# Kernel tuning notes

Hardware: AMD Instinct MI355X
Metric: run time of the kernel (lower is better)

Reference implementation:

```python
import jax, jax.numpy as jnp
import numpy as np

B = 4096
OBS_DIM = 1024
E_OUT = 512
H1 = 2048
H2 = 2048


def setup_inputs() -> dict:
    key = jax.random.key(0)
    ks = jax.random.split(key, 12)
    def kaiming(k, shape, fan_in):
        return jax.random.normal(k, shape, dtype=jnp.float32) * np.float32(np.sqrt(2.0 / fan_in))
    obs = jax.random.normal(ks[0], (B, OBS_DIM), dtype=jnp.float32)
    # lineare: Linear(obs_dim, e_outputs), torch weight shape [out, in]
    We = kaiming(ks[1], (E_OUT, OBS_DIM), OBS_DIM)
    be = jax.random.normal(ks[2], (E_OUT,), dtype=jnp.float32) * 0.01
    # obs_dim attention heads, each Linear(e_outputs, 2), stacked
    attn_W = kaiming(ks[3], (OBS_DIM, E_OUT, 2), E_OUT)
    attn_b = jax.random.normal(ks[4], (OBS_DIM, 2), dtype=jnp.float32) * 0.01
    # v_net: Linear(obs_dim,H1)+tanh, Linear(H1,H2)+[dropout(eval:no-op)]+tanh, Linear(H2,1)
    W1 = kaiming(ks[5], (H1, OBS_DIM), OBS_DIM)
    b1 = jnp.zeros((H1,), dtype=jnp.float32)
    W2 = kaiming(ks[6], (H2, H1), H1)
    b2 = jnp.zeros((H2,), dtype=jnp.float32)
    W3 = kaiming(ks[7], (1, H2), H2)
    b3 = jnp.zeros((1,), dtype=jnp.float32)
    return {"obs": obs, "We": We, "be": be, "attn_W": attn_W, "attn_b": attn_b,
            "W1": W1, "b1": b1, "W2": W2, "b2": b2, "W3": W3, "b3": b3}


def reference(obs, We, be, attn_W, attn_b, W1, b1, W2, b2, W3, b3):
    # e = tanh(lineare(obs)) : [B, E_OUT]
    e = jnp.tanh(obs @ We.T + be)
    # all obs_dim attention heads batched into one contraction: [B, OBS_DIM, 2]
    logits = jnp.einsum('be,oec->boc', e, attn_W) + attn_b
    # softmax over the 2 logits, keep prob of class 1 -> Attention [B, OBS_DIM]
    attention = jax.nn.softmax(logits, axis=-1)[..., 1]
    state_attention = obs * attention
    # v_net (eval mode: dropout is identity)
    h = jnp.tanh(state_attention @ W1.T + b1)
    h = jnp.tanh(h @ W2.T + b2)
    v = jnp.squeeze(h @ W3.T + b3, -1)  # [B]
    return (v, attention)
```

## Files before the change

### kernel.cpp

```cpp
#include <hip/hip_runtime.h>
#include <hip/hip_bf16.h>

typedef unsigned short u16;
typedef u16 u16x4 __attribute__((ext_vector_type(4)));
typedef u16 u16x8 __attribute__((ext_vector_type(8)));
typedef __bf16 bf16x8 __attribute__((ext_vector_type(8)));
typedef float f32x4 __attribute__((ext_vector_type(4)));

__device__ __forceinline__ u16 f2bf(float f) {
  unsigned u = __float_as_uint(f);
  u += 0x7FFFu + ((u >> 16) & 1u);
  return (u16)(u >> 16);
}
__device__ __forceinline__ float bf2f(u16 h) {
  return __uint_as_float(((unsigned)h) << 16);
}
__device__ __forceinline__ float tanh_fast(float x) {
  float t = __expf(2.0f * x);
  return 1.0f - 2.0f / (t + 1.0f);
}
__device__ __forceinline__ float sigmoid_fast(float x) {
  return 1.0f / (1.0f + __expf(-x));
}

__device__ __forceinline__ void glds16(const u16* g, u16* l) {
  __builtin_amdgcn_global_load_lds(
      (const __attribute__((address_space(1))) unsigned int*)g,
      (__attribute__((address_space(3))) unsigned int*)l, 16, 0, 0);
}

__device__ __forceinline__ void cvt4(const float* __restrict__ s, u16* __restrict__ d, int q) {
  float4 v = ((const float4*)s)[q];
  u16x4 o = { f2bf(v.x), f2bf(v.y), f2bf(v.z), f2bf(v.w) };
  ((u16x4*)d)[q] = o;
}

__global__ __launch_bounds__(256)
void prep_kernel(const float* __restrict__ obs, const float* __restrict__ We,
                 const float* __restrict__ W1, const float* __restrict__ W2,
                 const float* __restrict__ aW, const float* __restrict__ ab,
                 u16* __restrict__ obs_b, u16* __restrict__ We_b,
                 u16* __restrict__ W1_b, u16* __restrict__ W2_b,
                 u16* __restrict__ Wd, float* __restrict__ bd,
                 float* __restrict__ vzero) {
  int q = blockIdx.x * 256 + threadIdx.x;
  if (q < 1024) ((float4*)vzero)[q] = (float4){0.f, 0.f, 0.f, 0.f};
  if (q < 1048576) { cvt4(obs, obs_b, q); return; }
  q -= 1048576;
  if (q < 131072) { cvt4(We, We_b, q); return; }
  q -= 131072;
  if (q < 524288) { cvt4(W1, W1_b, q); return; }
  q -= 524288;
  if (q < 1048576) { cvt4(W2, W2_b, q); return; }
  q -= 1048576;
  if (q < 131072) {
    int i0 = q * 4;
    int o = i0 >> 9, e0 = i0 & 511;
    const float* p = aW + (size_t)o * 1024 + e0 * 2;
    float4 v0 = *(const float4*)p;
    float4 v1 = *(const float4*)(p + 4);
    u16x4 od = { f2bf(v0.y - v0.x), f2bf(v0.w - v0.z),
                 f2bf(v1.y - v1.x), f2bf(v1.w - v1.z) };
    *(u16x4*)(Wd + i0) = od;
    if (q < 256) {
      float4 a0 = *(const float4*)(ab + q * 8);
      float4 a1 = *(const float4*)(ab + q * 8 + 4);
      float4 ob = { a0.y - a0.x, a0.w - a0.z, a1.y - a1.x, a1.w - a1.z };
      *(float4*)(bd + q * 4) = ob;
    }
  }
}

template <int BM, int BN, int EP>
__global__ __launch_bounds__(256, 2)
void gemm_bt(const u16* __restrict__ A, const u16* __restrict__ Bt,
             int N, int K,
             const float* __restrict__ bias,
             u16* __restrict__ outb, float* __restrict__ outf,
             const u16* __restrict__ obsb, u16* __restrict__ sa,
             const float* __restrict__ W3, const float* __restrict__ b3,
             float* __restrict__ vout) {
  constexpr int CA = BM / 32;
  constexpr int CB = BN / 32;
  constexpr int MI = BM / 32;
  constexpr int NJ = BN / 32;

  __shared__ __align__(16) u16 As0[BM * 64];
  __shared__ __align__(16) u16 Bs0[BN * 64];
  __shared__ __align__(16) u16 As1[BM * 64];
  __shared__ __align__(16) u16 Bs1[BN * 64];

  const int tid = threadIdx.x;
  const int lane = tid & 63;
  const int wave = tid >> 6;
  const int bm = blockIdx.x, bn = blockIdx.y;

  const int r0 = tid >> 3;
  const int kcs = ((tid & 7) ^ (r0 & 7)) * 8;

  const u16* gA = A + (size_t)(bm * BM + r0) * K + kcs;
  const u16* gB = Bt + (size_t)(bn * BN + r0) * K + kcs;

  const int wm = (wave >> 1) * (BM / 2);
  const int wn = (wave & 1) * (BN / 2);
  const int fr = lane & 15;
  const int hi = lane >> 4;
  const int frx = fr & 7;

  f32x4 acc[MI][NJ];
#pragma unroll
  for (int i = 0; i < MI; ++i)
#pragma unroll
    for (int j = 0; j < NJ; ++j)
      acc[i][j] = (f32x4){0.f, 0.f, 0.f, 0.f};

  auto stage = [&](u16* __restrict__ dA, u16* __restrict__ dB) {
#pragma unroll
    for (int q = 0; q < CA; ++q)
      glds16(gA + (size_t)q * 32 * K, dA + tid * 8 + q * 2048);
#pragma unroll
    for (int q = 0; q < CB; ++q)
      glds16(gB + (size_t)q * 32 * K, dB + tid * 8 + q * 2048);
    gA += 64; gB += 64;
  };

  auto compute = [&](const u16* sA, const u16* sB) {
#pragma unroll
    for (int s = 0; s < 2; ++s) {
      const int ck = ((s * 4 + hi) ^ frx) * 8;
      bf16x8 a[MI], b[NJ];
#pragma unroll
      for (int i = 0; i < MI; ++i)
        a[i] = *(const bf16x8*)(sA + (wm + i * 16 + fr) * 64 + ck);
#pragma unroll
      for (int j = 0; j < NJ; ++j)
        b[j] = *(const bf16x8*)(sB + (wn + j * 16 + fr) * 64 + ck);
#pragma unroll
      for (int i = 0; i < MI; ++i)
#pragma unroll
        for (int j = 0; j < NJ; ++j)
          acc[i][j] = __builtin_amdgcn_mfma_f32_16x16x32_bf16(a[i], b[j], acc[i][j], 0, 0, 0);
    }
  };

  const int T = K >> 6;
  stage(As0, Bs0);
  __syncthreads();
  for (int k = 0; k < T; k += 2) {
    stage(As1, Bs1);
    compute(As0, Bs0);
    __syncthreads();
    if (k + 2 < T) stage(As0, Bs0);
    compute(As1, Bs1);
    __syncthreads();
  }

  if constexpr (EP == 2) {
    float vpart[MI][4];
#pragma unroll
    for (int i = 0; i < MI; ++i)
#pragma unroll
      for (int r = 0; r < 4; ++r) vpart[i][r] = 0.f;
#pragma unroll
    for (int j = 0; j < NJ; ++j) {
      const int col = bn * BN + wn + j * 16 + fr;
      const float bv = bias[col];
      const float w3 = W3[col];
#pragma unroll
      for (int i = 0; i < MI; ++i)
#pragma unroll
        for (int r = 0; r < 4; ++r)
          vpart[i][r] += tanh_fast(acc[i][j][r] + bv) * w3;
    }
    const bool lead = (fr == 0);
    const bool addb = (bn == 0) && ((wave & 1) == 0);
#pragma unroll
    for (int i = 0; i < MI; ++i)
#pragma unroll
      for (int r = 0; r < 4; ++r) {
        float p = vpart[i][r];
        p += __shfl_xor(p, 8);
        p += __shfl_xor(p, 4);
        p += __shfl_xor(p, 2);
        p += __shfl_xor(p, 1);
        if (lead) {
          const int row = bm * BM + wm + i * 16 + (lane >> 4) * 4 + r;
          atomicAdd(vout + row, addb ? p + b3[0] : p);
        }
      }
  } else {
#pragma unroll
    for (int j = 0; j < NJ; ++j) {
      const int col = bn * BN + wn + j * 16 + fr;
      const float bv = bias[col];
#pragma unroll
      for (int i = 0; i < MI; ++i) {
#pragma unroll
        for (int r = 0; r < 4; ++r) {
          const int row = bm * BM + wm + i * 16 + (lane >> 4) * 4 + r;
          const float x = acc[i][j][r] + bv;
          const size_t idx = (size_t)row * N + col;
          if constexpr (EP == 0) {
            outb[idx] = f2bf(tanh_fast(x));
          } else {
            const float att = sigmoid_fast(x);
            outf[idx] = att;
            sa[idx] = f2bf(bf2f(obsb[idx]) * att);
          }
        }
      }
    }
  }
}

extern "C" void kernel_launch(void* const* d_in, const int* in_sizes, int n_in,
                              void* d_out, int out_size, void* d_ws, size_t ws_size,
                              hipStream_t stream) {
  const float* obs   = (const float*)d_in[0];
  const float* We    = (const float*)d_in[1];
  const float* be    = (const float*)d_in[2];
  const float* attnW = (const float*)d_in[3];
  const float* attnb = (const float*)d_in[4];
  const float* W1    = (const float*)d_in[5];
  const float* b1    = (const float*)d_in[6];
  const float* W2    = (const float*)d_in[7];
  const float* b2    = (const float*)d_in[8];
  const float* W3    = (const float*)d_in[9];
  const float* b3    = (const float*)d_in[10];
  float* out = (float*)d_out;

  char* ws = (char*)d_ws;
  u16*   We_b  = (u16*)(ws + 0x00000000);
  u16*   Wd_b  = (u16*)(ws + 0x00100000);
  u16*   W1_b  = (u16*)(ws + 0x00200000);
  u16*   W2_b  = (u16*)(ws + 0x00600000);
  float* bd    = (float*)(ws + 0x00E00000);
  u16*   obs_b = (u16*)(ws + 0x00E01000);
  u16*   e_b   = (u16*)(ws + 0x01601000);
  u16*   sa_b  = (u16*)(ws + 0x01A01000);
  u16*   h1_b  = (u16*)(ws + 0x02201000);

  prep_kernel<<<11264, 256, 0, stream>>>(obs, We, W1, W2, attnW, attnb,
                                         obs_b, We_b, W1_b, W2_b, Wd_b, bd, out);

  gemm_bt<64, 64, 0><<<dim3(64, 8), 256, 0, stream>>>(
      obs_b, We_b, 512, 1024, be, e_b, nullptr, nullptr, nullptr, nullptr, nullptr, nullptr);
  gemm_bt<128, 64, 1><<<dim3(32, 16), 256, 0, stream>>>(
      e_b, Wd_b, 1024, 512, bd, nullptr, out + 4096, obs_b, sa_b, nullptr, nullptr, nullptr);
  gemm_bt<128, 128, 0><<<dim3(32, 16), 256, 0, stream>>>(
      sa_b, W1_b, 2048, 1024, b1, h1_b, nullptr, nullptr, nullptr, nullptr, nullptr, nullptr);
  gemm_bt<128, 128, 2><<<dim3(32, 16), 256, 0, stream>>>(
      h1_b, W2_b, 2048, 2048, b2, nullptr, nullptr, nullptr, nullptr, W3, b3, out);
}
```

Before: 189.9 us.

## Add 8-wave 4-stage pipelined GEMM kernel for the two large MLP layers

Introduces a gemm_big kernel with 512 threads, 128x128 tiles and a four-buffer LDS ring that issues loads three k-steps ahead. It uses a counted vmcnt wait with a single barrier per step and raises MFMA priority with s_setprio. The two large v_net GEMMs now run on this kernel, while gemm_bt keeps only the bf16/sigmoid epilogues. The aim is to hide global load latency better and overlap memory with MFMA work, at the cost of 128KB of LDS per block, which limits occupancy to one block per CU.

Result: slower. 206.2 us (+8.6%).

```diff
diff --git a/kernel.cpp b/kernel.cpp
--- a/kernel.cpp
+++ b/kernel.cpp
@@ -77,9 +77,7 @@
              int N, int K,
              const float* __restrict__ bias,
              u16* __restrict__ outb, float* __restrict__ outf,
-             const u16* __restrict__ obsb, u16* __restrict__ sa,
-             const float* __restrict__ W3, const float* __restrict__ b3,
-             float* __restrict__ vout) {
+             const u16* __restrict__ obsb, u16* __restrict__ sa) {
   constexpr int CA = BM / 32;
   constexpr int CB = BN / 32;
   constexpr int MI = BM / 32;
@@ -155,6 +153,129 @@
     __syncthreads();
   }
 
+#pragma unroll
+  for (int j = 0; j < NJ; ++j) {
+    const int col = bn * BN + wn + j * 16 + fr;
+    const float bv = bias[col];
+#pragma unroll
+    for (int i = 0; i < MI; ++i) {
+#pragma unroll
+      for (int r = 0; r < 4; ++r) {
+        const int row = bm * BM + wm + i * 16 + hi * 4 + r;
+        const float x = acc[i][j][r] + bv;
+        const size_t idx = (size_t)row * N + col;
+        if constexpr (EP == 0) {
+          outb[idx] = f2bf(tanh_fast(x));
+        } else {
+          const float att = sigmoid_fast(x);
+          outf[idx] = att;
+          sa[idx] = f2bf(bf2f(obsb[idx]) * att);
+        }
+      }
+    }
+  }
+}
+
+template <int EP>
+__global__ __launch_bounds__(512, 1)
+void gemm_big(const u16* __restrict__ A, const u16* __restrict__ Bt,
+              int N, int K,
+              const float* __restrict__ bias,
+              u16* __restrict__ outb,
+              const float* __restrict__ W3, const float* __restrict__ b3,
+              float* __restrict__ vout) {
+  constexpr int MI = 4;
+  constexpr int NJ = 2;
+
+  __shared__ __align__(16) u16 As0[8192], Bs0[8192];
+  __shared__ __align__(16) u16 As1[8192], Bs1[8192];
+  __shared__ __align__(16) u16 As2[8192], Bs2[8192];
+  __shared__ __align__(16) u16 As3[8192], Bs3[8192];
+
+  const int tid = threadIdx.x;
+  const int lane = tid & 63;
+  const int wave = tid >> 6;
+  const int bm = blockIdx.x, bn = blockIdx.y;
+
+  const int r0 = tid >> 3;
+  const int kcs = ((tid & 7) ^ (r0 & 7)) * 8;
+
+  const u16* gA0 = A + (size_t)(bm * 128 + r0) * K + kcs;
+  const u16* gA1 = gA0 + (size_t)64 * K;
+  const u16* gB0 = Bt + (size_t)(bn * 128 + r0) * K + kcs;
+  const u16* gB1 = gB0 + (size_t)64 * K;
+
+  const int wm = (wave >> 2) * 64;
+  const int wn = (wave & 3) * 32;
+  const int fr = lane & 15;
+  const int hi = lane >> 4;
+  const int frx = fr & 7;
+
+  f32x4 acc[MI][NJ];
+#pragma unroll
+  for (int i = 0; i < MI; ++i)
+#pragma unroll
+    for (int j = 0; j < NJ; ++j)
+      acc[i][j] = (f32x4){0.f, 0.f, 0.f, 0.f};
+
+  const int T = K >> 6;
+
+  auto stage = [&](int ts, u16* __restrict__ dA, u16* __restrict__ dB) {
+    const size_t o = (size_t)ts * 64;
+    glds16(gA0 + o, dA + tid * 8);
+    glds16(gA1 + o, dA + 4096 + tid * 8);
+    glds16(gB0 + o, dB + tid * 8);
+    glds16(gB1 + o, dB + 4096 + tid * 8);
+  };
+
+  auto compute = [&](const u16* sA, const u16* sB) {
+#pragma unroll
+    for (int s = 0; s < 2; ++s) {
+      const int ck = ((s * 4 + hi) ^ frx) * 8;
+      bf16x8 a[MI], b[NJ];
+#pragma unroll
+      for (int j = 0; j < NJ; ++j)
+        b[j] = *(const bf16x8*)(sB + (wn + j * 16 + fr) * 64 + ck);
+#pragma unroll
+      for (int i = 0; i < MI; ++i)
+        a[i] = *(const bf16x8*)(sA + (wm + i * 16 + fr) * 64 + ck);
+      __builtin_amdgcn_s_setprio(1);
+#pragma unroll
+      for (int i = 0; i < MI; ++i)
+#pragma unroll
+        for (int j = 0; j < NJ; ++j)
+          acc[i][j] = __builtin_amdgcn_mfma_f32_16x16x32_bf16(a[i], b[j], acc[i][j], 0, 0, 0);
+      __builtin_amdgcn_s_setprio(0);
+    }
+  };
+
+  stage(0, As0, Bs0);
+  stage(1, As1, Bs1);
+  stage(2, As2, Bs2);
+
+#define SLOT(t, Ac, Bc, Asg, Bsg)                                   \
+  do {                                                              \
+    asm volatile("s_waitcnt vmcnt(8)" ::: "memory");                \
+    __builtin_amdgcn_sched_barrier(0);                              \
+    __builtin_amdgcn_s_barrier();                                   \
+    __builtin_amdgcn_sched_barrier(0);                              \
+    {                                                               \
+      int ts = (t) + 3; if (ts > T - 1) ts = T - 1;                 \
+      stage(ts, Asg, Bsg);                                          \
+    }                                                               \
+    compute(Ac, Bc);                                                \
+  } while (0)
+
+  for (int m = 0; m < T; m += 4) {
+    SLOT(m + 0, As0, Bs0, As3, Bs3);
+    SLOT(m + 1, As1, Bs1, As0, Bs0);
+    SLOT(m + 2, As2, Bs2, As1, Bs1);
+    SLOT(m + 3, As3, Bs3, As2, Bs2);
+  }
+#undef SLOT
+
+  asm volatile("s_waitcnt vmcnt(0)" ::: "memory");
+
   if constexpr (EP == 2) {
     float vpart[MI][4];
 #pragma unroll
@@ -163,7 +284,7 @@
       for (int r = 0; r < 4; ++r) vpart[i][r] = 0.f;
 #pragma unroll
     for (int j = 0; j < NJ; ++j) {
-      const int col = bn * BN + wn + j * 16 + fr;
+      const int col = bn * 128 + wn + j * 16 + fr;
       const float bv = bias[col];
       const float w3 = W3[col];
 #pragma unroll
@@ -173,7 +294,7 @@
           vpart[i][r] += tanh_fast(acc[i][j][r] + bv) * w3;
     }
     const bool lead = (fr == 0);
-    const bool addb = (bn == 0) && ((wave & 1) == 0);
+    const bool addb = (bn == 0) && ((wave & 3) == 0);
 #pragma unroll
     for (int i = 0; i < MI; ++i)
 #pragma unroll
@@ -184,29 +305,21 @@
         p += __shfl_xor(p, 2);
         p += __shfl_xor(p, 1);
         if (lead) {
-          const int row = bm * BM + wm + i * 16 + (lane >> 4) * 4 + r;
+          const int row = bm * 128 + wm + i * 16 + hi * 4 + r;
           atomicAdd(vout + row, addb ? p + b3[0] : p);
         }
       }
   } else {
 #pragma unroll
     for (int j = 0; j < NJ; ++j) {
-      const int col = bn * BN + wn + j * 16 + fr;
+      const int col = bn * 128 + wn + j * 16 + fr;
       const float bv = bias[col];
 #pragma unroll
       for (int i = 0; i < MI; ++i) {
 #pragma unroll
         for (int r = 0; r < 4; ++r) {
-          const int row = bm * BM + wm + i * 16 + (lane >> 4) * 4 + r;
-          const float x = acc[i][j][r] + bv;
-          const size_t idx = (size_t)row * N + col;
-          if constexpr (EP == 0) {
-            outb[idx] = f2bf(tanh_fast(x));
-          } else {
-            const float att = sigmoid_fast(x);
-            outf[idx] = att;
-            sa[idx] = f2bf(bf2f(obsb[idx]) * att);
-          }
+          const int row = bm * 128 + wm + i * 16 + hi * 4 + r;
+          outb[(size_t)row * N + col] = f2bf(tanh_fast(acc[i][j][r] + bv));
         }
       }
     }
@@ -244,11 +357,11 @@
                                          obs_b, We_b, W1_b, W2_b, Wd_b, bd, out);
 
   gemm_bt<64, 64, 0><<<dim3(64, 8), 256, 0, stream>>>(
-      obs_b, We_b, 512, 1024, be, e_b, nullptr, nullptr, nullptr, nullptr, nullptr, nullptr);
+      obs_b, We_b, 512, 1024, be, e_b, nullptr, nullptr, nullptr);
   gemm_bt<128, 64, 1><<<dim3(32, 16), 256, 0, stream>>>(
-      e_b, Wd_b, 1024, 512, bd, nullptr, out + 4096, obs_b, sa_b, nullptr, nullptr, nullptr);
-  gemm_bt<128, 128, 0><<<dim3(32, 16), 256, 0, stream>>>(
-      sa_b, W1_b, 2048, 1024, b1, h1_b, nullptr, nullptr, nullptr, nullptr, nullptr, nullptr);
-  gemm_bt<128, 128, 2><<<dim3(32, 16), 256, 0, stream>>>(
-      h1_b, W2_b, 2048, 2048, b2, nullptr, nullptr, nullptr, nullptr, W3, b3, out);
-}
+      e_b, Wd_b, 1024, 512, bd, nullptr, out + 4096, obs_b, sa_b);
+  gemm_big<0><<<dim3(32, 16), 512, 0, stream>>>(
+      sa_b, W1_b, 2048, 1024, b1, h1_b, nullptr, nullptr, nullptr);
+  gemm_big<2><<<dim3(32, 16), 512, 0, stream>>>(
+      h1_b, W2_b, 2048, 2048, b2, nullptr, W3, b3, out);
+}
```

## Load A operand fragments directly from global into registers, stage only B in LDS

Applied to the files above, without the earlier changes.

The A tile is no longer staged through shared memory. Each wave now loads its own MFMA A fragments straight from global memory into registers, double-buffered one k-tile ahead, and only the B tile still goes through LDS. This halves or more the LDS footprint and removes the A LDS reads. In exchange the two waves that share the same rows fetch A redundantly, the 16-byte loads are strided per row, and register pressure rises, which may limit occupancy or expose global latency.

Measured after the change: 282.3 us. +48.6%, slower.

```diff
diff --git a/kernel.cpp b/kernel.cpp
--- a/kernel.cpp
+++ b/kernel.cpp
@@ -80,14 +80,11 @@
              const u16* __restrict__ obsb, u16* __restrict__ sa,
              const float* __restrict__ W3, const float* __restrict__ b3,
              float* __restrict__ vout) {
-  constexpr int CA = BM / 32;
   constexpr int CB = BN / 32;
   constexpr int MI = BM / 32;
   constexpr int NJ = BN / 32;
 
-  __shared__ __align__(16) u16 As0[BM * 64];
   __shared__ __align__(16) u16 Bs0[BN * 64];
-  __shared__ __align__(16) u16 As1[BM * 64];
   __shared__ __align__(16) u16 Bs1[BN * 64];
 
   const int tid = threadIdx.x;
@@ -98,7 +95,6 @@
   const int r0 = tid >> 3;
   const int kcs = ((tid & 7) ^ (r0 & 7)) * 8;
 
-  const u16* gA = A + (size_t)(bm * BM + r0) * K + kcs;
   const u16* gB = Bt + (size_t)(bn * BN + r0) * K + kcs;
 
   const int wm = (wave >> 1) * (BM / 2);
@@ -107,6 +103,11 @@
   const int hi = lane >> 4;
   const int frx = fr & 7;
 
+  const u16* pA[MI];
+#pragma unroll
+  for (int i = 0; i < MI; ++i)
+    pA[i] = A + (size_t)(bm * BM + wm + i * 16 + fr) * K + hi * 8;
+
   f32x4 acc[MI][NJ];
 #pragma unroll
   for (int i = 0; i < MI; ++i)
@@ -114,24 +115,27 @@
     for (int j = 0; j < NJ; ++j)
       acc[i][j] = (f32x4){0.f, 0.f, 0.f, 0.f};
 
-  auto stage = [&](u16* __restrict__ dA, u16* __restrict__ dB) {
-#pragma unroll
-    for (int q = 0; q < CA; ++q)
-      glds16(gA + (size_t)q * 32 * K, dA + tid * 8 + q * 2048);
+  auto stageB = [&](u16* __restrict__ dB) {
 #pragma unroll
     for (int q = 0; q < CB; ++q)
       glds16(gB + (size_t)q * 32 * K, dB + tid * 8 + q * 2048);
-    gA += 64; gB += 64;
+    gB += 64;
   };
 
-  auto compute = [&](const u16* sA, const u16* sB) {
+  bf16x8 aP[MI][2], aQ[MI][2];
+  auto loadA = [&](bf16x8 (*dst)[2], int kt) {
+#pragma unroll
+    for (int i = 0; i < MI; ++i)
+#pragma unroll
+      for (int s = 0; s < 2; ++s)
+        dst[i][s] = *(const bf16x8*)(pA[i] + (size_t)kt * 64 + s * 32);
+  };
+
+  auto compute = [&](const bf16x8 (*af)[2], const u16* sB) {
 #pragma unroll
     for (int s = 0; s < 2; ++s) {
       const int ck = ((s * 4 + hi) ^ frx) * 8;
-      bf16x8 a[MI], b[NJ];
-#pragma unroll
-      for (int i = 0; i < MI; ++i)
-        a[i] = *(const bf16x8*)(sA + (wm + i * 16 + fr) * 64 + ck);
+      bf16x8 b[NJ];
 #pragma unroll
       for (int j = 0; j < NJ; ++j)
         b[j] = *(const bf16x8*)(sB + (wn + j * 16 + fr) * 64 + ck);
@@ -139,19 +143,21 @@
       for (int i = 0; i < MI; ++i)
 #pragma unroll
         for (int j = 0; j < NJ; ++j)
-          acc[i][j] = __builtin_amdgcn_mfma_f32_16x16x32_bf16(a[i], b[j], acc[i][j], 0, 0, 0);
+          acc[i][j] = __builtin_amdgcn_mfma_f32_16x16x32_bf16(af[i][s], b[j], acc[i][j], 0, 0, 0);
     }
   };
 
   const int T = K >> 6;
-  stage(As0, Bs0);
+  stageB(Bs0);
+  loadA(aP, 0);
   __syncthreads();
   for (int k = 0; k < T; k += 2) {
-    stage(As1, Bs1);
-    compute(As0, Bs0);
+    stageB(Bs1);
+    loadA(aQ, k + 1);
+    compute(aP, Bs0);
     __syncthreads();
-    if (k + 2 < T) stage(As0, Bs0);
-    compute(As1, Bs1);
+    if (k + 2 < T) { stageB(Bs0); loadA(aP, k + 2); }
+    compute(aQ, Bs1);
     __syncthreads();
   }
 
@@ -184,7 +190,7 @@
         p += __shfl_xor(p, 2);
         p += __shfl_xor(p, 1);
         if (lead) {
-          const int row = bm * BM + wm + i * 16 + (lane >> 4) * 4 + r;
+          const int row = bm * BM + wm + i * 16 + hi * 4 + r;
           atomicAdd(vout + row, addb ? p + b3[0] : p);
         }
       }
@@ -197,7 +203,7 @@
       for (int i = 0; i < MI; ++i) {
 #pragma unroll
         for (int r = 0; r < 4; ++r) {
-          const int row = bm * BM + wm + i * 16 + (lane >> 4) * 4 + r;
+          const int row = bm * BM + wm + i * 16 + hi * 4 + r;
           const float x = acc[i][j][r] + bv;
           const size_t idx = (size_t)row * N + col;
           if constexpr (EP == 0) {
```

## Add triple-buffered K32 GEMM kernel with fine-grained waitcnt for final layer

Applied to the files above, without the earlier changes.

Replaces the last GEMM (h1 x W2 with the fused tanh/W3 reduction) with a dedicated kernel. It uses 32-wide K tiles, three LDS buffers and explicit s_waitcnt vmcnt plus raw s_barrier, so global-to-LDS loads run two stages ahead of the MFMA compute. The fused value-head epilogue is moved into this kernel, and the generic GEMM loses its EP==2 path. The gain relies on deeper load/compute overlap; the risks are more barriers per K and hand-tuned wait counts that could race if they are wrong.

Result: slower. 196.5 us (+3.5%).

```diff
diff --git a/kernel.cpp b/kernel.cpp
--- a/kernel.cpp
+++ b/kernel.cpp
@@ -77,9 +77,7 @@
              int N, int K,
              const float* __restrict__ bias,
              u16* __restrict__ outb, float* __restrict__ outf,
-             const u16* __restrict__ obsb, u16* __restrict__ sa,
-             const float* __restrict__ W3, const float* __restrict__ b3,
-             float* __restrict__ vout) {
+             const u16* __restrict__ obsb, u16* __restrict__ sa) {
   constexpr int CA = BM / 32;
   constexpr int CB = BN / 32;
   constexpr int MI = BM / 32;
@@ -155,62 +153,136 @@
     __syncthreads();
   }
 
-  if constexpr (EP == 2) {
-    float vpart[MI][4];
-#pragma unroll
-    for (int i = 0; i < MI; ++i)
-#pragma unroll
-      for (int r = 0; r < 4; ++r) vpart[i][r] = 0.f;
-#pragma unroll
-    for (int j = 0; j < NJ; ++j) {
-      const int col = bn * BN + wn + j * 16 + fr;
-      const float bv = bias[col];
-      const float w3 = W3[col];
-#pragma unroll
-      for (int i = 0; i < MI; ++i)
-#pragma unroll
-        for (int r = 0; r < 4; ++r)
-          vpart[i][r] += tanh_fast(acc[i][j][r] + bv) * w3;
-    }
-    const bool lead = (fr == 0);
-    const bool addb = (bn == 0) && ((wave & 1) == 0);
-#pragma unroll
-    for (int i = 0; i < MI; ++i)
+#pragma unroll
+  for (int j = 0; j < NJ; ++j) {
+    const int col = bn * BN + wn + j * 16 + fr;
+    const float bv = bias[col];
+#pragma unroll
+    for (int i = 0; i < MI; ++i) {
 #pragma unroll
       for (int r = 0; r < 4; ++r) {
-        float p = vpart[i][r];
-        p += __shfl_xor(p, 8);
-        p += __shfl_xor(p, 4);
-        p += __shfl_xor(p, 2);
-        p += __shfl_xor(p, 1);
-        if (lead) {
-          const int row = bm * BM + wm + i * 16 + (lane >> 4) * 4 + r;
-          atomicAdd(vout + row, addb ? p + b3[0] : p);
-        }
-      }
-  } else {
-#pragma unroll
-    for (int j = 0; j < NJ; ++j) {
-      const int col = bn * BN + wn + j * 16 + fr;
-      const float bv = bias[col];
-#pragma unroll
-      for (int i = 0; i < MI; ++i) {
-#pragma unroll
-        for (int r = 0; r < 4; ++r) {
-          const int row = bm * BM + wm + i * 16 + (lane >> 4) * 4 + r;
-          const float x = acc[i][j][r] + bv;
-          const size_t idx = (size_t)row * N + col;
-          if constexpr (EP == 0) {
-            outb[idx] = f2bf(tanh_fast(x));
-          } else {
-            const float att = sigmoid_fast(x);
-            outf[idx] = att;
-            sa[idx] = f2bf(bf2f(obsb[idx]) * att);
-          }
+        const int row = bm * BM + wm + i * 16 + hi * 4 + r;
+        const float x = acc[i][j][r] + bv;
+        const size_t idx = (size_t)row * N + col;
+        if constexpr (EP == 0) {
+          outb[idx] = f2bf(tanh_fast(x));
+        } else {
+          const float att = sigmoid_fast(x);
+          outf[idx] = att;
+          sa[idx] = f2bf(bf2f(obsb[idx]) * att);
         }
       }
     }
   }
+}
+
+__global__ __launch_bounds__(256, 2)
+void gemm_k32v(const u16* __restrict__ A, const u16* __restrict__ Bt,
+               int K,
+               const float* __restrict__ bias,
+               const float* __restrict__ W3, const float* __restrict__ b3,
+               float* __restrict__ vout) {
+  __shared__ __align__(16) u16 As0[4096], Bs0[4096];
+  __shared__ __align__(16) u16 As1[4096], Bs1[4096];
+  __shared__ __align__(16) u16 As2[4096], Bs2[4096];
+
+  const int tid = threadIdx.x;
+  const int lane = tid & 63;
+  const int wave = tid >> 6;
+  const int bm = blockIdx.x, bn = blockIdx.y;
+
+  const int r0 = tid >> 2;
+  const int kcs = ((tid & 3) ^ (r0 & 3)) * 8;
+  const u16* gA = A + (size_t)(bm * 128 + r0) * K + kcs;
+  const u16* gB = Bt + (size_t)(bn * 128 + r0) * K + kcs;
+
+  const int wm = (wave >> 1) * 64;
+  const int wn = (wave & 1) * 64;
+  const int fr = lane & 15;
+  const int hi = lane >> 4;
+  const int ck = (hi ^ (fr & 3)) * 8;
+
+  f32x4 acc[4][4];
+#pragma unroll
+  for (int i = 0; i < 4; ++i)
+#pragma unroll
+    for (int j = 0; j < 4; ++j)
+      acc[i][j] = (f32x4){0.f, 0.f, 0.f, 0.f};
+
+  auto stage = [&](int ts, u16* __restrict__ dA, u16* __restrict__ dB) {
+    const size_t o = (size_t)ts * 32;
+    glds16(gA + o, dA + tid * 8);
+    glds16(gA + o + (size_t)64 * K, dA + 2048 + tid * 8);
+    glds16(gB + o, dB + tid * 8);
+    glds16(gB + o + (size_t)64 * K, dB + 2048 + tid * 8);
+  };
+
+  auto compute = [&](const u16* sA, const u16* sB) {
+    bf16x8 a[4], b[4];
+#pragma unroll
+    for (int j = 0; j < 4; ++j)
+      b[j] = *(const bf16x8*)(sB + (wn + j * 16 + fr) * 32 + ck);
+#pragma unroll
+    for (int i = 0; i < 4; ++i)
+      a[i] = *(const bf16x8*)(sA + (wm + i * 16 + fr) * 32 + ck);
+#pragma unroll
+    for (int i = 0; i < 4; ++i)
+#pragma unroll
+      for (int j = 0; j < 4; ++j)
+        acc[i][j] = __builtin_amdgcn_mfma_f32_16x16x32_bf16(a[i], b[j], acc[i][j], 0, 0, 0);
+  };
+
+  auto waitb = [] {
+    asm volatile("s_waitcnt vmcnt(4) lgkmcnt(0)" ::: "memory");
+    __builtin_amdgcn_sched_barrier(0);
+    __builtin_amdgcn_s_barrier();
+    __builtin_amdgcn_sched_barrier(0);
+  };
+
+  const int T = K >> 5;
+  stage(0, As0, Bs0);
+  stage(1, As1, Bs1);
+  waitb();
+  for (int t = 0; t < T - 1; t += 3) {
+    stage(t + 2 < T ? t + 2 : T - 1, As2, Bs2); compute(As0, Bs0); waitb();
+    stage(t + 3 < T ? t + 3 : T - 1, As0, Bs0); compute(As1, Bs1); waitb();
+    stage(t + 4 < T ? t + 4 : T - 1, As1, Bs1); compute(As2, Bs2); waitb();
+  }
+  compute(As0, Bs0);
+  asm volatile("s_waitcnt vmcnt(0)" ::: "memory");
+
+  float vpart[4][4];
+#pragma unroll
+  for (int i = 0; i < 4; ++i)
+#pragma unroll
+    for (int r = 0; r < 4; ++r) vpart[i][r] = 0.f;
+#pragma unroll
+  for (int j = 0; j < 4; ++j) {
+    const int col = bn * 128 + wn + j * 16 + fr;
+    const float bv = bias[col];
+    const float w3 = W3[col];
+#pragma unroll
+    for (int i = 0; i < 4; ++i)
+#pragma unroll
+      for (int r = 0; r < 4; ++r)
+        vpart[i][r] += tanh_fast(acc[i][j][r] + bv) * w3;
+  }
+  const bool lead = (fr == 0);
+  const bool addb = (bn == 0) && ((wave & 1) == 0);
+#pragma unroll
+  for (int i = 0; i < 4; ++i)
+#pragma unroll
+    for (int r = 0; r < 4; ++r) {
+      float p = vpart[i][r];
+      p += __shfl_xor(p, 8);
+      p += __shfl_xor(p, 4);
+      p += __shfl_xor(p, 2);
+      p += __shfl_xor(p, 1);
+      if (lead) {
+        const int row = bm * 128 + wm + i * 16 + hi * 4 + r;
+        atomicAdd(vout + row, addb ? p + b3[0] : p);
+      }
+    }
 }
 
 extern "C" void kernel_launch(void* const* d_in, const int* in_sizes, int n_in,
@@ -244,11 +316,11 @@
                                          obs_b, We_b, W1_b, W2_b, Wd_b, bd, out);
 
   gemm_bt<64, 64, 0><<<dim3(64, 8), 256, 0, stream>>>(
-      obs_b, We_b, 512, 1024, be, e_b, nullptr, nullptr, nullptr, nullptr, nullptr, nullptr);
+      obs_b, We_b, 512, 1024, be, e_b, nullptr, nullptr, nullptr);
   gemm_bt<128, 64, 1><<<dim3(32, 16), 256, 0, stream>>>(
-      e_b, Wd_b, 1024, 512, bd, nullptr, out + 4096, obs_b, sa_b, nullptr, nullptr, nullptr);
+      e_b, Wd_b, 1024, 512, bd, nullptr, out + 4096, obs_b, sa_b);
   gemm_bt<128, 128, 0><<<dim3(32, 16), 256, 0, stream>>>(
-      sa_b, W1_b, 2048, 1024, b1, h1_b, nullptr, nullptr, nullptr, nullptr, nullptr, nullptr);
-  gemm_bt<128, 128, 2><<<dim3(32, 16), 256, 0, stream>>>(
-      h1_b, W2_b, 2048, 2048, b2, nullptr, nullptr, nullptr, nullptr, W3, b3, out);
-}
+      sa_b, W1_b, 2048, 1024, b1, h1_b, nullptr, nullptr, nullptr);
+  gemm_k32v<<<dim3(32, 16), 256, 0, stream>>>(
+      h1_b, W2_b, 2048, b2, W3, b3, out);
+}
```
